# Kernel optimization log

Hardware: AMD Instinct MI355X
Metric: run time of the kernel (lower is better)

The kernel has to match this reference:

```python
import jax, jax.numpy as jnp
import numpy as np

N, C, T, V = 32, 256, 256, 25
CI = C // 2
BN_EPS = 1e-5


def setup_inputs() -> dict:
    key = jax.random.key(0)
    ks = jax.random.split(key, 11)
    s = 1.0 / np.sqrt(C)
    si = 1.0 / np.sqrt(CI)
    return {
        "x": jax.random.normal(ks[0], (N, C, T, V), dtype=jnp.float32),
        "Wg": jax.random.normal(ks[1], (CI, C), dtype=jnp.float32) * s,
        "bg": jax.random.normal(ks[2], (CI,), dtype=jnp.float32) * s,
        "Wth": jax.random.normal(ks[3], (CI, C), dtype=jnp.float32) * s,
        "bth": jax.random.normal(ks[4], (CI,), dtype=jnp.float32) * s,
        "Wph": jax.random.normal(ks[5], (CI, C), dtype=jnp.float32) * s,
        "bph": jax.random.normal(ks[6], (CI,), dtype=jnp.float32) * s,
        "Ww": jax.random.normal(ks[7], (C, CI), dtype=jnp.float32) * si,
        "bw": jax.random.normal(ks[8], (C,), dtype=jnp.float32) * si,
        "gamma": jax.random.normal(ks[9], (C,), dtype=jnp.float32) * 0.1,
        "beta": jax.random.normal(ks[10], (C,), dtype=jnp.float32) * 0.1,
    }


def reference(x, Wg, bg, Wth, bth, Wph, bph, Ww, bw, gamma, beta):
    n, c, t, v = x.shape
    ci = Wg.shape[0]
    # [N,C,T,V] -> [N*V, C, T] (permute(0,3,1,2).reshape)
    xf = jnp.transpose(x, (0, 3, 1, 2)).reshape(n * v, c, t)
    # 1x1 Conv1d == channel GEMM
    g_x = jnp.einsum('bct,oc->bot', xf, Wg) + bg[:, None]      # [N*V, Ci, T]
    g_x = g_x.reshape(n, v * ci, t).transpose(0, 2, 1)         # [N, T, V*Ci]
    xmean = xf.reshape(n, v, c, t).mean(axis=1)                # [N, C, T]
    theta = (jnp.einsum('nct,oc->not', xmean, Wth) + bth[:, None]).transpose(0, 2, 1)  # [N,T,Ci]
    phi = jnp.einsum('nct,oc->not', xmean, Wph) + bph[:, None]  # [N, Ci, T]
    f = jnp.matmul(theta, phi)                                  # [N, T, T]
    f = jax.nn.softmax(f, axis=-1)
    y = jnp.matmul(f, g_x)                                      # [N, T, V*Ci]
    y = y.transpose(0, 2, 1).reshape(n * v, ci, t)              # [N*V, Ci, T]
    wy = jnp.einsum('bct,oc->bot', y, Ww) + bw[:, None]         # [N*V, C, T]
    # BatchNorm1d (training mode: batch stats over (batch, T))
    mu = wy.mean(axis=(0, 2))
    var = wy.var(axis=(0, 2))
    wy = (wy - mu[:, None]) * jax.lax.rsqrt(var[:, None] + BN_EPS) * gamma[:, None] + beta[:, None]
    z = wy + xf                                                 # residual
    return jnp.transpose(z.reshape(n, v, c, t), (0, 2, 3, 1))   # [N, C, T, V]
```

## Files before the change

### kernel.cpp

```cpp
#include <hip/hip_runtime.h>

typedef unsigned short u16;
using s8v = __attribute__((ext_vector_type(8))) short;
using f4v = __attribute__((ext_vector_type(4))) float;

constexpr int kN = 32, kC = 256, kT = 256, kV = 25, kCI = 128;
constexpr int kTV = kT * kV;
constexpr int kCIV = kCI * kV;
constexpr int kSAMP = kN * kT * kV;
constexpr int SYY_B = 256;

__device__ __forceinline__ float bf2f(u16 v) {
  return __uint_as_float(((unsigned)v) << 16);
}
__device__ __forceinline__ u16 f2bf(float f) {
  unsigned u = __float_as_uint(f);
  return (u16)((u + 0x7FFFu + ((u >> 16) & 1u)) >> 16);
}

__global__ __launch_bounds__(256) void k_prep(const float* __restrict__ x, u16* __restrict__ x_bf,
                                              float* __restrict__ xm) {
  __shared__ float sm[6400];
  size_t base = (size_t)blockIdx.x * 6400;
  const float4* src = (const float4*)(x + base);
  ushort4* dst = (ushort4*)(x_bf + base);
  for (int i = threadIdx.x; i < 1600; i += 256) {
    float4 v = src[i];
    ((float4*)sm)[i] = v;
    ushort4 b;
    b.x = f2bf(v.x); b.y = f2bf(v.y); b.z = f2bf(v.z); b.w = f2bf(v.w);
    dst[i] = b;
  }
  __syncthreads();
  const float* r = sm + threadIdx.x * 25;
  float s = 0.f;
#pragma unroll
  for (int j = 0; j < 25; ++j) s += r[j];
  xm[(size_t)blockIdx.x * 256 + threadIdx.x] = s * (1.0f / kV);
}

__global__ __launch_bounds__(256) void k_cvtW(const float* __restrict__ Wg, const float* __restrict__ Ww,
                                              const float* __restrict__ Wth, const float* __restrict__ Wph,
                                              u16* __restrict__ Wg_fl, u16* __restrict__ Ww_fl,
                                              u16* __restrict__ Wthph_fl) {
  int i = blockIdx.x * 256 + threadIdx.x;
  { int m = i >> 8, k = i & 255; Wg_fl[(size_t)((k >> 3) * 128 + m) * 8 + (k & 7)] = f2bf(Wg[i]); }
  { int m = i >> 7, k = i & 127; Ww_fl[(size_t)((k >> 3) * 256 + m) * 8 + (k & 7)] = f2bf(Ww[i]); }
  { int m = i >> 8, k = i & 255;
    Wthph_fl[(size_t)((k >> 3) * 256 + m) * 8 + (k & 7)] = f2bf(Wth[i]);
    Wthph_fl[(size_t)((k >> 3) * 256 + (m + 128)) * 8 + (k & 7)] = f2bf(Wph[i]); }
}

__global__ __launch_bounds__(512) void k_fattn(const float* __restrict__ xmean,
                                               const u16* __restrict__ Wthph_fl,
                                               const float* __restrict__ bth, const float* __restrict__ bph,
                                               u16* __restrict__ f) {
  __shared__ __align__(16) u16 lds[49152];
  const int n = blockIdx.x >> 1, tc0 = (blockIdx.x & 1) * 128;
  const int tid = threadIdx.x, lane = tid & 63, w = tid >> 6;
  const int l15 = lane & 15, l4 = lane >> 4;
  const int wro = (w & 3) * 64, wct = (w >> 2) * 128;
  f4v acc[4][8];
#pragma unroll
  for (int i = 0; i < 4; ++i)
#pragma unroll
    for (int j = 0; j < 8; ++j) acc[i][j] = f4v{0.f, 0.f, 0.f, 0.f};
  for (int ch = 0; ch < 2; ++ch) {
    __syncthreads();
    for (int e = tid; e < 8192; e += 512) {
      int cc = e >> 6, t4 = (e & 63) * 4;
      float4 v = *(const float4*)(xmean + (((size_t)(n * 256 + ch * 128 + cc)) << 8) + t4);
      u16* d = &lds[(((cc >> 3) * 256 + t4) << 3) + (cc & 7)];
      d[0] = f2bf(v.x); d[8] = f2bf(v.y); d[16] = f2bf(v.z); d[24] = f2bf(v.w);
    }
    __syncthreads();
#pragma unroll
    for (int ks = 0; ks < 4; ++ks) {
      const int ksub = ks * 4 + l4;
      s8v af[4], bf[8];
#pragma unroll
      for (int fi = 0; fi < 4; ++fi)
        af[fi] = *(const s8v*)(Wthph_fl + (size_t)((ch * 16 + ksub) * 256 + wro + fi * 16 + l15) * 8);
#pragma unroll
      for (int g = 0; g < 8; ++g)
        bf[g] = *(const s8v*)&lds[((ksub * 256 + wct + g * 16 + l15) << 3)];
#pragma unroll
      for (int g = 0; g < 8; ++g)
#pragma unroll
        for (int fi = 0; fi < 4; ++fi)
          acc[fi][g] = __builtin_amdgcn_mfma_f32_16x16x32_bf16(af[fi], bf[g], acc[fi][g], 0, 0, 0);
    }
  }
  __syncthreads();
#pragma unroll
  for (int fi = 0; fi < 4; ++fi) {
    int o0 = wro + fi * 16 + l4 * 4;
    bool isTh = o0 < 128;
    float bb[4];
#pragma unroll
    for (int r = 0; r < 4; ++r) bb[r] = isTh ? bth[o0 + r] : bph[o0 - 128 + r];
#pragma unroll
    for (int g = 0; g < 8; ++g) {
      int t = wct + g * 16 + l15;
      ushort4 pk;
      pk.x = f2bf(acc[fi][g][0] + bb[0]);
      pk.y = f2bf(acc[fi][g][1] + bb[1]);
      pk.z = f2bf(acc[fi][g][2] + bb[2]);
      pk.w = f2bf(acc[fi][g][3] + bb[3]);
      if (isTh) {
        unsigned tl = (unsigned)(t - tc0);
        if (tl < 128u)
          *(ushort4*)&lds[(((o0 >> 3) * 128 + (int)tl) << 3) + (o0 & 7)] = pk;
      } else {
        int o = o0 - 128;
        *(ushort4*)&lds[16384 + (((o >> 3) * 256 + t) << 3) + (o & 7)] = pk;
      }
    }
  }
  __syncthreads();
  const int wr = (w & 3) * 64, wcc = (w >> 2) * 64;
  const int wM = w & 3;
  f4v facc[4][4];
#pragma unroll
  for (int i = 0; i < 4; ++i)
#pragma unroll
    for (int j = 0; j < 4; ++j) facc[i][j] = f4v{0.f, 0.f, 0.f, 0.f};
#pragma unroll
  for (int ks = 0; ks < 4; ++ks) {
    const int ksub = ks * 4 + l4;
    s8v af[4], bf[4];
#pragma unroll
    for (int fi = 0; fi < 4; ++fi)
      af[fi] = *(const s8v*)&lds[16384 + ((ksub * 256 + wr + fi * 16 + l15) << 3)];
#pragma unroll
    for (int g = 0; g < 4; ++g)
      bf[g] = *(const s8v*)&lds[((ksub * 128 + wcc + g * 16 + l15) << 3)];
#pragma unroll
    for (int g = 0; g < 4; ++g)
#pragma unroll
      for (int fi = 0; fi < 4; ++fi)
        facc[fi][g] = __builtin_amdgcn_mfma_f32_16x16x32_bf16(af[fi], bf[g], facc[fi][g], 0, 0, 0);
  }
  __syncthreads();
  float* redm = (float*)lds;
  float* reds = redm + 512;
  float mx[4], sm[4];
#pragma unroll
  for (int g = 0; g < 4; ++g) {
    float m = -1e30f;
#pragma unroll
    for (int fi = 0; fi < 4; ++fi)
#pragma unroll
      for (int r = 0; r < 4; ++r) m = fmaxf(m, facc[fi][g][r]);
    m = fmaxf(m, __shfl_xor(m, 16));
    m = fmaxf(m, __shfl_xor(m, 32));
    mx[g] = m;
  }
  if (l4 == 0)
#pragma unroll
    for (int g = 0; g < 4; ++g) redm[wM * 128 + wcc + g * 16 + l15] = mx[g];
  __syncthreads();
#pragma unroll
  for (int g = 0; g < 4; ++g) {
    int col = wcc + g * 16 + l15;
    mx[g] = fmaxf(fmaxf(redm[col], redm[128 + col]), fmaxf(redm[256 + col], redm[384 + col]));
  }
#pragma unroll
  for (int g = 0; g < 4; ++g) {
    float s = 0.f;
#pragma unroll
    for (int fi = 0; fi < 4; ++fi)
#pragma unroll
      for (int r = 0; r < 4; ++r) {
        float e = __expf(facc[fi][g][r] - mx[g]);
        facc[fi][g][r] = e;
        s += e;
      }
    s += __shfl_xor(s, 16);
    s += __shfl_xor(s, 32);
    sm[g] = s;
  }
  if (l4 == 0)
#pragma unroll
    for (int g = 0; g < 4; ++g) reds[wM * 128 + wcc + g * 16 + l15] = sm[g];
  __syncthreads();
#pragma unroll
  for (int g = 0; g < 4; ++g) {
    int col = wcc + g * 16 + l15;
    float inv = 1.0f / (reds[col] + reds[128 + col] + reds[256 + col] + reds[384 + col]);
    int t = tc0 + col;
#pragma unroll
    for (int fi = 0; fi < 4; ++fi) {
      int tp0 = wr + fi * 16 + l4 * 4;
      ushort4 st;
      st.x = f2bf(facc[fi][g][0] * inv);
      st.y = f2bf(facc[fi][g][1] * inv);
      st.z = f2bf(facc[fi][g][2] * inv);
      st.w = f2bf(facc[fi][g][3] * inv);
      *(ushort4*)(f + (size_t)(n * 256 + t) * 256 + tp0) = st;
    }
  }
}

template <int K_TOT, int NCOLS, int MODE, int NT>
__global__ __launch_bounds__(NT) void k_gemm(
    const u16* __restrict__ A_, const u16* __restrict__ B_, const float* __restrict__ bias,
    void* __restrict__ outp, const float* __restrict__ scale, const float* __restrict__ shift,
    const u16* __restrict__ xres) {
  constexpr int KSTEPS = K_TOT / 32;
  constexpr int M_TOT = (MODE == 0) ? 128 : 256;
  __shared__ uint4 Bs[512];
  const int n = blockIdx.z, m0 = blockIdx.y * ((NT == 512) ? 256 : 128), n0 = blockIdx.x * 128;
  const int tid = threadIdx.x, lane = tid & 63, w = tid >> 6;
  const int wr = (w >> 1) * 64, wc = (w & 1) * 64;
  const int l15 = lane & 15, l4 = lane >> 4;
  const u16* Bn = B_ + (size_t)n * K_TOT * NCOLS + n0;
  const int scol = tid & 127, sk0 = tid >> 7;
  f4v acc[4][4];
#pragma unroll
  for (int i = 0; i < 4; ++i)
#pragma unroll
    for (int j = 0; j < 4; ++j) acc[i][j] = f4v{0.f, 0.f, 0.f, 0.f};

  for (int ks = 0; ks < KSTEPS; ++ks) {
    __syncthreads();
#pragma unroll
    for (int p = 0; p < 512 / NT; ++p) {
      int ksub = sk0 + p * (NT / 128);
      const u16* src = Bn + (size_t)(ks * 32 + ksub * 8) * NCOLS + scol;
      union { u16 u[8]; uint4 v; } pk;
#pragma unroll
      for (int j = 0; j < 8; ++j) pk.u[j] = src[(size_t)j * NCOLS];
      int blk = ksub * 128 + scol;
      blk ^= (blk >> 2) & 3;
      Bs[blk] = pk.v;
    }
    __syncthreads();
    s8v af[4];
#pragma unroll
    for (int fi = 0; fi < 4; ++fi) {
      int m = m0 + wr + fi * 16 + l15;
      const u16* ap;
      if constexpr (MODE == 1)
        ap = A_ + ((size_t)(n * 256 + m) * 256 + ks * 32 + l4 * 8);
      else
        ap = A_ + (size_t)((ks * 4 + l4) * M_TOT + m) * 8;
      af[fi] = *(const s8v*)ap;
    }
#pragma unroll
    for (int g = 0; g < 4; ++g) {
      int blk = l4 * 128 + wc + g * 16 + l15;
      blk ^= (blk >> 2) & 3;
      s8v bf = *(const s8v*)&Bs[blk];
#pragma unroll
      for (int fi = 0; fi < 4; ++fi)
        acc[fi][g] = __builtin_amdgcn_mfma_f32_16x16x32_bf16(af[fi], bf, acc[fi][g], 0, 0, 0);
    }
  }
#pragma unroll
  for (int fi = 0; fi < 4; ++fi) {
    int growb = m0 + wr + fi * 16 + l4 * 4;
#pragma unroll
    for (int g = 0; g < 4; ++g) {
      int gcol = n0 + wc + g * 16 + l15;
#pragma unroll
      for (int r = 0; r < 4; ++r) {
        int grow = growb + r;
        float vv = acc[fi][g][r];
        if constexpr (MODE == 0) {
          vv += bias[grow];
          int t = gcol / 25, v5 = gcol - t * 25;
          ((u16*)outp)[((size_t)n * kT + t) * kCIV + grow * 25 + v5] = f2bf(vv);
        } else if constexpr (MODE == 1) {
          int ci = gcol / 25, v5 = gcol - ci * 25;
          ((u16*)outp)[((size_t)n * kCI + ci) * kTV + grow * 25 + v5] = f2bf(vv);
        } else {
          size_t idx = ((size_t)n * kC + grow) * kTV + gcol;
          ((float*)outp)[idx] = vv * scale[grow] + shift[grow] + bf2f(xres[idx]);
        }
      }
    }
  }
}

__global__ __launch_bounds__(256) void k_syy(const u16* __restrict__ yb, float* __restrict__ psyy,
                                             float* __restrict__ psy) {
  const int b = blockIdx.x, n = b >> 3, kc = b & 7;
  const int kbase = kc * 800;
  const int tid = threadIdx.x, lane = tid & 63, w = tid >> 6;
  const int wr = (w >> 1) * 64, wc = (w & 1) * 64, l15 = lane & 15, l4 = lane >> 4;
  const u16* Y = yb + (size_t)n * kCI * kTV;
  f4v acc[4][4];
#pragma unroll
  for (int i = 0; i < 4; ++i)
#pragma unroll
    for (int j = 0; j < 4; ++j) acc[i][j] = f4v{0.f, 0.f, 0.f, 0.f};
  float syl[4] = {0.f, 0.f, 0.f, 0.f};
  for (int ks = 0; ks < 25; ++ks) {
    int k = kbase + ks * 32 + l4 * 8;
    s8v af[4], bf[4];
#pragma unroll
    for (int fi = 0; fi < 4; ++fi) {
      af[fi] = *(const s8v*)(Y + (size_t)(wr + fi * 16 + l15) * kTV + k);
      bf[fi] = *(const s8v*)(Y + (size_t)(wc + fi * 16 + l15) * kTV + k);
    }
#pragma unroll
    for (int fi = 0; fi < 4; ++fi)
#pragma unroll
      for (int j = 0; j < 8; ++j) syl[fi] += bf2f((u16)af[fi][j]);
#pragma unroll
    for (int g = 0; g < 4; ++g)
#pragma unroll
      for (int fi = 0; fi < 4; ++fi)
        acc[fi][g] = __builtin_amdgcn_mfma_f32_16x16x32_bf16(af[fi], bf[g], acc[fi][g], 0, 0, 0);
  }
  float* pb = psyy + (size_t)b * 16384;
#pragma unroll
  for (int fi = 0; fi < 4; ++fi)
#pragma unroll
    for (int g = 0; g < 4; ++g)
#pragma unroll
      for (int r = 0; r < 4; ++r)
        pb[(wr + fi * 16 + l4 * 4 + r) * kCI + wc + g * 16 + l15] = acc[fi][g][r];
#pragma unroll
  for (int fi = 0; fi < 4; ++fi) {
    float s = syl[fi];
    s += __shfl_xor(s, 16);
    s += __shfl_xor(s, 32);
    if ((w & 1) == 0 && l4 == 0) psy[b * kCI + wr + fi * 16 + l15] = s;
  }
}

__global__ __launch_bounds__(256) void k_reduce(const float* __restrict__ psyy, const float* __restrict__ psy,
                                                float* __restrict__ syy, float* __restrict__ sy) {
  if (blockIdx.x < 64) {
    int i = blockIdx.x * 256 + threadIdx.x;
    float s = 0.f;
    for (int b = 0; b < SYY_B; ++b) s += psyy[(size_t)b * 16384 + i];
    syy[i] = s;
  } else if (threadIdx.x < kCI) {
    float s = 0.f;
    for (int b = 0; b < SYY_B; ++b) s += psy[b * kCI + threadIdx.x];
    sy[threadIdx.x] = s;
  }
}

__global__ __launch_bounds__(128) void k_stats(const float* __restrict__ syy, const float* __restrict__ sy,
                                               const float* __restrict__ Ww, const float* __restrict__ bw,
                                               const float* __restrict__ gamma, const float* __restrict__ beta,
                                               float* __restrict__ scale, float* __restrict__ shift) {
  int c2 = blockIdx.x;
  int tid = threadIdx.x;
  __shared__ float wsm[kCI];
  __shared__ float red1[kCI], red2[kCI];
  wsm[tid] = Ww[c2 * kCI + tid];
  __syncthreads();
  float val = 0.f;
#pragma unroll 8
  for (int ci = 0; ci < kCI; ++ci) val = fmaf(wsm[ci], syy[ci * kCI + tid], val);
  red1[tid] = wsm[tid] * sy[tid];
  red2[tid] = val * wsm[tid];
  __syncthreads();
  for (int s = 64; s > 0; s >>= 1) {
    if (tid < s) { red1[tid] += red1[tid + s]; red2[tid] += red2[tid + s]; }
    __syncthreads();
  }
  if (tid == 0) {
    const float invS = 1.0f / (float)kSAMP;
    float m1 = red1[0] * invS;
    float b = bw[c2];
    float mu = m1 + b;
    float e2 = red2[0] * invS + 2.f * b * m1 + b * b;
    float var = e2 - mu * mu;
    float rstd = rsqrtf(var + 1e-5f);
    float sc = rstd * gamma[c2];
    scale[c2] = sc;
    shift[c2] = beta[c2] + (b - mu) * sc;
  }
}

extern "C" void kernel_launch(void* const* d_in, const int* in_sizes, int n_in,
                              void* d_out, int out_size, void* d_ws, size_t ws_size,
                              hipStream_t stream) {
  const float* x     = (const float*)d_in[0];
  const float* Wg    = (const float*)d_in[1];
  const float* bg    = (const float*)d_in[2];
  const float* Wth   = (const float*)d_in[3];
  const float* bth   = (const float*)d_in[4];
  const float* Wph   = (const float*)d_in[5];
  const float* bph   = (const float*)d_in[6];
  const float* Ww    = (const float*)d_in[7];
  const float* bw    = (const float*)d_in[8];
  const float* gamma = (const float*)d_in[9];
  const float* beta  = (const float*)d_in[10];
  float* out = (float*)d_out;

  char* wsb = (char*)d_ws;
  float* xmean = (float*)(wsb);
  u16* Wthph_fl = (u16*)(wsb + (8u << 20));
  u16*   f_bf  = (u16*)(wsb + (12u << 20));
  float* psy   = (float*)(wsb + (16u << 20));
  float* syy   = (float*)(wsb + (17u << 20));
  float* sy    = syy + 16384;
  float* scale = sy + 128;
  float* shift = scale + 256;
  u16* Wg_fl = (u16*)(wsb + (18u << 20));
  u16* Ww_fl = Wg_fl + 32768;
  u16* x_bf  = (u16*)(wsb + (19u << 20));
  u16* g2    = (u16*)(wsb + (119u << 20));
  float* psyy = (float*)(wsb + (119u << 20));
  u16* yb    = (u16*)(wsb + (172u << 20));

  k_cvtW<<<128, 256, 0, stream>>>(Wg, Ww, Wth, Wph, Wg_fl, Ww_fl, Wthph_fl);
  k_prep<<<8192, 256, 0, stream>>>(x, x_bf, xmean);
  k_fattn<<<64, 512, 0, stream>>>(xmean, Wthph_fl, bth, bph, f_bf);
  k_gemm<256, kTV, 0, 256><<<dim3(50, 1, 32), 256, 0, stream>>>(
      Wg_fl, x_bf, bg, (void*)g2, nullptr, nullptr, nullptr);
  k_gemm<256, kCIV, 1, 512><<<dim3(25, 1, 32), 512, 0, stream>>>(
      f_bf, g2, nullptr, (void*)yb, nullptr, nullptr, nullptr);
  k_syy<<<SYY_B, 256, 0, stream>>>(yb, psyy, psy);
  k_reduce<<<65, 256, 0, stream>>>(psyy, psy, syy, sy);
  k_stats<<<256, 128, 0, stream>>>(syy, sy, Ww, bw, gamma, beta, scale, shift);
  k_gemm<128, kTV, 2, 512><<<dim3(50, 1, 32), 512, 0, stream>>>(
      Ww_fl, yb, nullptr, (void*)out, scale, shift, x_bf);
}
```

Baseline: 352.1 us.

## Fuse weight conversion into prep, widen reduce parallelism, add gemm occupancy hint

```diff
diff --git a/kernel.cpp b/kernel.cpp
--- a/kernel.cpp
+++ b/kernel.cpp
@@ -19,8 +19,21 @@
 }
 
 __global__ __launch_bounds__(256) void k_prep(const float* __restrict__ x, u16* __restrict__ x_bf,
-                                              float* __restrict__ xm) {
+                                              float* __restrict__ xm,
+                                              const float* __restrict__ Wg, const float* __restrict__ Ww,
+                                              const float* __restrict__ Wth, const float* __restrict__ Wph,
+                                              u16* __restrict__ Wg_fl, u16* __restrict__ Ww_fl,
+                                              u16* __restrict__ Wthph_fl) {
   __shared__ float sm[6400];
+  if (blockIdx.x >= 8192) {
+    int i = (blockIdx.x - 8192) * 256 + threadIdx.x;
+    { int m = i >> 8, k = i & 255; Wg_fl[(size_t)((k >> 3) * 128 + m) * 8 + (k & 7)] = f2bf(Wg[i]); }
+    { int m = i >> 7, k = i & 127; Ww_fl[(size_t)((k >> 3) * 256 + m) * 8 + (k & 7)] = f2bf(Ww[i]); }
+    { int m = i >> 8, k = i & 255;
+      Wthph_fl[(size_t)((k >> 3) * 256 + m) * 8 + (k & 7)] = f2bf(Wth[i]);
+      Wthph_fl[(size_t)((k >> 3) * 256 + (m + 128)) * 8 + (k & 7)] = f2bf(Wph[i]); }
+    return;
+  }
   size_t base = (size_t)blockIdx.x * 6400;
   const float4* src = (const float4*)(x + base);
   ushort4* dst = (ushort4*)(x_bf + base);
@@ -37,18 +50,6 @@
 #pragma unroll
   for (int j = 0; j < 25; ++j) s += r[j];
   xm[(size_t)blockIdx.x * 256 + threadIdx.x] = s * (1.0f / kV);
-}
-
-__global__ __launch_bounds__(256) void k_cvtW(const float* __restrict__ Wg, const float* __restrict__ Ww,
-                                              const float* __restrict__ Wth, const float* __restrict__ Wph,
-                                              u16* __restrict__ Wg_fl, u16* __restrict__ Ww_fl,
-                                              u16* __restrict__ Wthph_fl) {
-  int i = blockIdx.x * 256 + threadIdx.x;
-  { int m = i >> 8, k = i & 255; Wg_fl[(size_t)((k >> 3) * 128 + m) * 8 + (k & 7)] = f2bf(Wg[i]); }
-  { int m = i >> 7, k = i & 127; Ww_fl[(size_t)((k >> 3) * 256 + m) * 8 + (k & 7)] = f2bf(Ww[i]); }
-  { int m = i >> 8, k = i & 255;
-    Wthph_fl[(size_t)((k >> 3) * 256 + m) * 8 + (k & 7)] = f2bf(Wth[i]);
-    Wthph_fl[(size_t)((k >> 3) * 256 + (m + 128)) * 8 + (k & 7)] = f2bf(Wph[i]); }
 }
 
 __global__ __launch_bounds__(512) void k_fattn(const float* __restrict__ xmean,
@@ -203,7 +204,7 @@
 }
 
 template <int K_TOT, int NCOLS, int MODE, int NT>
-__global__ __launch_bounds__(NT) void k_gemm(
+__global__ __launch_bounds__(NT, 4) void k_gemm(
     const u16* __restrict__ A_, const u16* __restrict__ B_, const float* __restrict__ bias,
     void* __restrict__ outp, const float* __restrict__ scale, const float* __restrict__ shift,
     const u16* __restrict__ xres) {
@@ -333,15 +334,23 @@
 
 __global__ __launch_bounds__(256) void k_reduce(const float* __restrict__ psyy, const float* __restrict__ psy,
                                                 float* __restrict__ syy, float* __restrict__ sy) {
-  if (blockIdx.x < 64) {
-    int i = blockIdx.x * 256 + threadIdx.x;
+  if (blockIdx.x < 256) {
+    int i = blockIdx.x * 64 + (threadIdx.x >> 2);
+    int part = threadIdx.x & 3;
     float s = 0.f;
-    for (int b = 0; b < SYY_B; ++b) s += psyy[(size_t)b * 16384 + i];
-    syy[i] = s;
-  } else if (threadIdx.x < kCI) {
+    for (int b = part; b < SYY_B; b += 4) s += psyy[(size_t)b * 16384 + i];
+    s += __shfl_xor(s, 1);
+    s += __shfl_xor(s, 2);
+    if (part == 0) syy[i] = s;
+  } else {
+    int c = threadIdx.x & 127;
+    int half = threadIdx.x >> 7;
     float s = 0.f;
-    for (int b = 0; b < SYY_B; ++b) s += psy[b * kCI + threadIdx.x];
-    sy[threadIdx.x] = s;
+    for (int b = half; b < SYY_B; b += 2) s += psy[b * kCI + c];
+    __shared__ float tmp[128];
+    if (half == 1) tmp[c] = s;
+    __syncthreads();
+    if (half == 0) sy[c] = s + tmp[c];
   }
 }
 
@@ -411,15 +420,14 @@
   float* psyy = (float*)(wsb + (119u << 20));
   u16* yb    = (u16*)(wsb + (172u << 20));
 
-  k_cvtW<<<128, 256, 0, stream>>>(Wg, Ww, Wth, Wph, Wg_fl, Ww_fl, Wthph_fl);
-  k_prep<<<8192, 256, 0, stream>>>(x, x_bf, xmean);
+  k_prep<<<8320, 256, 0, stream>>>(x, x_bf, xmean, Wg, Ww, Wth, Wph, Wg_fl, Ww_fl, Wthph_fl);
   k_fattn<<<64, 512, 0, stream>>>(xmean, Wthph_fl, bth, bph, f_bf);
   k_gemm<256, kTV, 0, 256><<<dim3(50, 1, 32), 256, 0, stream>>>(
       Wg_fl, x_bf, bg, (void*)g2, nullptr, nullptr, nullptr);
   k_gemm<256, kCIV, 1, 512><<<dim3(25, 1, 32), 512, 0, stream>>>(
       f_bf, g2, nullptr, (void*)yb, nullptr, nullptr, nullptr);
   k_syy<<<SYY_B, 256, 0, stream>>>(yb, psyy, psy);
-  k_reduce<<<65, 256, 0, stream>>>(psyy, psy, syy, sy);
+  k_reduce<<<257, 256, 0, stream>>>(psyy, psy, syy, sy);
   k_stats<<<256, 128, 0, stream>>>(syy, sy, Ww, bw, gamma, beta, scale, shift);
   k_gemm<128, kTV, 2, 512><<<dim3(50, 1, 32), 512, 0, stream>>>(
       Ww_fl, yb, nullptr, (void*)out, scale, shift, x_bf);
```

Measured after the change: 369.3 us. +4.9%, slower.
